# Optimization experiments

Hardware: AMD Instinct MI355X
Metric: run time of the kernel (lower is better)

Reference implementation:

```python
import jax, jax.numpy as jnp
import numpy as np

B, C_IN, C_OUT, IMG, K_STEPS = 32, 64, 8, 128, 8


def setup_inputs() -> dict:
    key = jax.random.key(0)
    k1, k2, k3, k4, k5 = jax.random.split(key, 5)
    x = jax.random.normal(k1, (B, C_IN, IMG, IMG), dtype=jnp.float32)
    rand_pixel = jax.random.uniform(k2, (B, 1, IMG, IMG), dtype=jnp.float32)
    conv_w = jax.random.normal(k3, (C_OUT, C_IN), dtype=jnp.float32) * (1.0 / np.sqrt(C_IN))
    conv_b = jax.random.normal(k4, (C_OUT,), dtype=jnp.float32) * 0.01
    gate = jax.random.normal(k5, (), dtype=jnp.float32)
    # gaussian kernel init: sigma = 1 / (K_steps * log 2)
    log_sigma = jnp.asarray(np.log(1.0 / (K_STEPS * np.log(2.0))), dtype=jnp.float32)
    return {"x": x, "rand_pixel": rand_pixel, "conv_w": conv_w, "conv_b": conv_b,
            "gate": gate, "log_sigma": log_sigma}


def _semiconv(x, conv_w, conv_b, gate):
    # 1x1 conv == channel contraction
    out = gate * (jnp.einsum('oc,bchw->bohw', conv_w, x) + conv_b[None, :, None, None])
    B_, Cout, H, W = out.shape
    g1, g2 = jnp.meshgrid(jnp.linspace(-1.0, 1.0, H), jnp.linspace(-1.0, 1.0, W), indexing='ij')
    coords = jnp.stack([g1, g2])[None].astype(out.dtype)          # [1,2,H,W]
    uv = jnp.concatenate([jnp.zeros((1, Cout - 2, H, W), out.dtype), coords], axis=1)
    return out + uv


def reference(x, rand_pixel, conv_w, conv_b, gate, log_sigma):
    Bsz, _, H, W = x.shape
    feat = _semiconv(x, conv_w, conv_b, gate)              # [B,Cout,H,W]
    Cout = feat.shape[1]
    feat_flat = feat.reshape(Bsz, Cout, H * W)
    sigma = jnp.exp(log_sigma)

    def step(log_scope, _):
        # seed pixel selection: argmax of rand * scope over image
        pixel_probs = rand_pixel * jnp.exp(log_scope)       # [B,1,H,W]
        flat_idx = jnp.argmax(pixel_probs.reshape(Bsz, -1), axis=1)   # [B]
        seed = jnp.take_along_axis(feat_flat, flat_idx[:, None, None], axis=2)  # [B,Cout,1]
        sq_dist = jnp.sum((feat_flat - seed) ** 2, axis=1).reshape(Bsz, 1, H, W)
        alpha = jnp.exp(-sq_dist / sigma)                   # gaussian kernel
        # straight-through clamp to [0.01, 0.99]
        alpha = alpha + jax.lax.stop_gradient(jnp.clip(alpha, 0.01, 0.99) - alpha)
        log_m = log_scope + jnp.log(alpha)
        new_scope = log_scope + jnp.log1p(-alpha)
        return new_scope, (log_m, new_scope)

    log_scope0 = jnp.zeros((Bsz, 1, H, W), feat.dtype)
    final_scope, (lms, lss) = jax.lax.scan(step, log_scope0, None, length=K_STEPS - 1)
    # lms/lss: [K-1,B,1,H,W]
    log_masks = jnp.concatenate([lms, final_scope[None]], axis=0)   # last mask = final scope
    log_scopes = jnp.concatenate([log_scope0[None], lss], axis=0)
    log_masks = jnp.moveaxis(log_masks[:, :, 0], 0, 1)    # [B,K,H,W]
    log_scopes = jnp.moveaxis(log_scopes[:, :, 0], 0, 1)  # [B,K,H,W]
    return log_masks, log_scopes
```

## Files before the change

### kernel.cpp

```cpp
#include <hip/hip_runtime.h>

#define C_IN 64
#define C_OUT 8
#define IMG 128
#define HW (IMG * IMG)
#define BATCH 32
#define K_STEPS 8

#define FEAT_BYTES ((size_t)BATCH * HW * C_OUT * 4)
#define BLK_PER_B 8
#define NFLAGS ((K_STEPS - 1) * BATCH * BLK_PER_B)
#define NSEED0 (BATCH * 16)

union F2U { float2 f2; unsigned long long u; };

__global__ __launch_bounds__(256) void semiconv_kernel(
    const float* __restrict__ x,
    const float* __restrict__ w,
    const float* __restrict__ bias,
    const float* __restrict__ gate_p,
    const float* __restrict__ rand_pixel,
    float* __restrict__ feat,
    unsigned long long* __restrict__ flags,
    unsigned long long* __restrict__ seed0)
{
    __shared__ float sw[C_OUT * C_IN];
    __shared__ float spv[4];
    __shared__ int   spi[4];
    const int tid = threadIdx.x;
    if (blockIdx.x == 0) {
        for (int k = tid; k < NFLAGS; k += 256) flags[k] = 0ULL;
    }
    for (int i = tid; i < C_OUT * C_IN; i += 256) sw[i] = w[i];
    __syncthreads();

    const int b     = blockIdx.x >> 4;
    const int blk16 = blockIdx.x & 15;
    const int p4    = ((blk16 * 256) + tid) * 4;

    const float gate = *gate_p;
    const float* xb = x + (long long)b * C_IN * HW + p4;

    float acc[C_OUT][4];
    #pragma unroll
    for (int o = 0; o < C_OUT; ++o) {
        const float bv = bias[o];
        #pragma unroll
        for (int j = 0; j < 4; ++j) acc[o][j] = bv;
    }

    for (int c = 0; c < C_IN; ++c) {
        const float4 xv = *(const float4*)(xb + c * HW);
        const float xs[4] = {xv.x, xv.y, xv.z, xv.w};
        #pragma unroll
        for (int o = 0; o < C_OUT; ++o) {
            const float wv = sw[o * C_IN + c];
            #pragma unroll
            for (int j = 0; j < 4; ++j) acc[o][j] = fmaf(wv, xs[j], acc[o][j]);
        }
    }

    const int row  = p4 / IMG;
    const int col0 = p4 % IMG;
    const float step = 2.0f / (IMG - 1);
    const float g1 = -1.0f + step * (float)row;

    float* dst = feat + ((long long)b * HW + p4) * C_OUT;
    #pragma unroll
    for (int j = 0; j < 4; ++j) {
        float o0 = gate * acc[0][j];
        float o1 = gate * acc[1][j];
        float o2 = gate * acc[2][j];
        float o3 = gate * acc[3][j];
        float o4 = gate * acc[4][j];
        float o5 = gate * acc[5][j];
        float o6 = gate * acc[6][j] + g1;
        float o7 = gate * acc[7][j] + (-1.0f + step * (float)(col0 + j));
        *(float4*)(dst + j * C_OUT)     = make_float4(o0, o1, o2, o3);
        *(float4*)(dst + j * C_OUT + 4) = make_float4(o4, o5, o6, o7);
    }

    const int lane = tid & 63;
    const int wid  = tid >> 6;
    const float4 rv = *(const float4*)(rand_pixel + (size_t)b * HW + p4);
    float bv = rv.x; int bi = p4;
    if (rv.y > bv) { bv = rv.y; bi = p4 + 1; }
    if (rv.z > bv) { bv = rv.z; bi = p4 + 2; }
    if (rv.w > bv) { bv = rv.w; bi = p4 + 3; }
    #pragma unroll
    for (int off = 1; off < 64; off <<= 1) {
        const float ov = __shfl_xor(bv, off);
        const int   oi = __shfl_xor(bi, off);
        if (ov > bv || (ov == bv && oi < bi)) { bv = ov; bi = oi; }
    }
    if (lane == 0) { spv[wid] = bv; spi[wid] = bi; }
    __syncthreads();
    if (tid == 0) {
        float v = spv[0]; int ix = spi[0];
        #pragma unroll
        for (int wv2 = 1; wv2 < 4; ++wv2) {
            if (spv[wv2] > v || (spv[wv2] == v && spi[wv2] < ix)) { v = spv[wv2]; ix = spi[wv2]; }
        }
        seed0[(b << 4) | blk16] =
            ((unsigned long long)__float_as_uint(v) << 32) |
            (unsigned long long)(unsigned int)ix;
    }
}

#define NT 1024
#define CHUNK (HW / BLK_PER_B)

__device__ __forceinline__ void nt_store2(float* p, float a, float bfl) {
    F2U v; v.f2 = make_float2(a, bfl);
    __builtin_nontemporal_store(v.u, (unsigned long long*)p);
}

__global__ __launch_bounds__(NT) void stick_kernel(
    const float* __restrict__ feat,
    const float* __restrict__ rand_pixel,
    const float* __restrict__ log_sigma_p,
    float* __restrict__ masks,
    float* __restrict__ scopes,
    unsigned long long* __restrict__ flags,
    const unsigned long long* __restrict__ seed0)
{
    const int b    = blockIdx.x & 31;
    const int blk  = blockIdx.x >> 5;
    const int tid  = threadIdx.x;
    const int lane = tid & 63;
    const int wid  = tid >> 6;

    const float inv_sigma = expf(-(*log_sigma_p));

    const float* fb = feat + (size_t)b * HW * C_OUT;
    const float* rb = rand_pixel + (size_t)b * HW;
    float* mb = masks  + (size_t)b * (K_STEPS * HW);
    float* sb = scopes + (size_t)b * (K_STEPS * HW);

    const int p0 = blk * CHUNK + 2 * tid;

    const float4 f0a = *(const float4*)(fb + (size_t)p0 * C_OUT);
    const float4 f0b = *(const float4*)(fb + (size_t)p0 * C_OUT + 4);
    const float4 f1a = *(const float4*)(fb + (size_t)p0 * C_OUT + 8);
    const float4 f1b = *(const float4*)(fb + (size_t)p0 * C_OUT + 12);

    const float2 rr = *(const float2*)(rb + p0);
    float ls0 = 0.0f, ls1 = 0.0f;
    nt_store2(sb + p0, 0.0f, 0.0f);

    __shared__ float swv[2][16];
    __shared__ int   swi[2][16];
    __shared__ int   sSeed[2];

    for (int s = 0; s < K_STEPS - 1; ++s) {
        const int par = s & 1;
        int seedIdx;

        if (s == 0) {
            float gv = -1.0f; int gi = 0x7fffffff;
            if (lane < 16) {
                const unsigned long long got = seed0[(b << 4) | lane];
                gv = __uint_as_float((unsigned int)(got >> 32));
                gi = (int)(unsigned int)(got & 0xffffffffULL);
            }
            #pragma unroll
            for (int off = 1; off < 16; off <<= 1) {
                const float ov = __shfl_xor(gv, off);
                const int   oi = __shfl_xor(gi, off);
                if (ov > gv || (ov == gv && oi < gi)) { gv = ov; gi = oi; }
            }
            seedIdx = __shfl(gi, 0);
        } else {
            const int recbase = (s * BATCH + b) * BLK_PER_B;

            float bv; int bi;
            {
                const float v0 = rr.x * expf(ls0);
                const float v1 = rr.y * expf(ls1);
                bv = v0; bi = p0;
                if (v1 > bv) { bv = v1; bi = p0 + 1; }
            }
            #pragma unroll
            for (int off = 1; off < 64; off <<= 1) {
                const float ov = __shfl_xor(bv, off);
                const int   oi = __shfl_xor(bi, off);
                if (ov > bv || (ov == bv && oi < bi)) { bv = ov; bi = oi; }
            }
            if (lane == 0) { swv[par][wid] = bv; swi[par][wid] = bi; }
            __syncthreads();

            if (wid == 0) {
                float v = (lane < 16) ? swv[par][lane] : -1.0f;
                int   ix = (lane < 16) ? swi[par][lane] : 0x7fffffff;
                #pragma unroll
                for (int off = 1; off < 16; off <<= 1) {
                    const float ov = __shfl_xor(v, off);
                    const int   oi = __shfl_xor(ix, off);
                    if (ov > v || (ov == v && oi < ix)) { v = ov; ix = oi; }
                }
                if (lane == 0) {
                    const unsigned long long pk =
                        ((unsigned long long)__float_as_uint(v) << 32) |
                        (unsigned long long)(unsigned int)(ix + 1);
                    __hip_atomic_store(&flags[recbase + blk], pk,
                                       __ATOMIC_RELAXED, __HIP_MEMORY_SCOPE_AGENT);
                }
                float gv = -1.0f; int gi = 0x7fffffff;
                if (lane < BLK_PER_B) {
                    unsigned long long got;
                    do {
                        got = __hip_atomic_load(&flags[recbase + lane],
                                                __ATOMIC_RELAXED,
                                                __HIP_MEMORY_SCOPE_AGENT);
                    } while (got == 0ULL);
                    gv = __uint_as_float((unsigned int)(got >> 32));
                    gi = (int)(unsigned int)(got & 0xffffffffULL) - 1;
                }
                #pragma unroll
                for (int off = 1; off < 8; off <<= 1) {
                    const float ov = __shfl_xor(gv, off);
                    const int   oi = __shfl_xor(gi, off);
                    if (ov > gv || (ov == gv && oi < gi)) { gv = ov; gi = oi; }
                }
                if (lane == 0) sSeed[par] = gi;
            }
            __syncthreads();
            seedIdx = sSeed[par];
        }

        const float4 s0 = *(const float4*)(fb + (size_t)seedIdx * C_OUT);
        const float4 s1 = *(const float4*)(fb + (size_t)seedIdx * C_OUT + 4);

        float sq0 = 0.0f, sq1 = 0.0f, d;
        d = f0a.x - s0.x; sq0 += d * d;
        d = f0a.y - s0.y; sq0 += d * d;
        d = f0a.z - s0.z; sq0 += d * d;
        d = f0a.w - s0.w; sq0 += d * d;
        d = f0b.x - s1.x; sq0 += d * d;
        d = f0b.y - s1.y; sq0 += d * d;
        d = f0b.z - s1.z; sq0 += d * d;
        d = f0b.w - s1.w; sq0 += d * d;
        d = f1a.x - s0.x; sq1 += d * d;
        d = f1a.y - s0.y; sq1 += d * d;
        d = f1a.z - s0.z; sq1 += d * d;
        d = f1a.w - s0.w; sq1 += d * d;
        d = f1b.x - s1.x; sq1 += d * d;
        d = f1b.y - s1.y; sq1 += d * d;
        d = f1b.z - s1.z; sq1 += d * d;
        d = f1b.w - s1.w; sq1 += d * d;

        float m0, m1;
        {
            const float t = sq0 * inv_sigma;
            float alpha = expf(-t);
            float log_a;
            if (alpha >= 0.99f)      { alpha = 0.99f; log_a = -0.010050336f; }
            else if (alpha <= 0.01f) { alpha = 0.01f; log_a = -4.6051702f;  }
            else                     { log_a = -t; }
            m0 = ls0 + log_a;
            ls0 += log1pf(-alpha);
        }
        {
            const float t = sq1 * inv_sigma;
            float alpha = expf(-t);
            float log_a;
            if (alpha >= 0.99f)      { alpha = 0.99f; log_a = -0.010050336f; }
            else if (alpha <= 0.01f) { alpha = 0.01f; log_a = -4.6051702f;  }
            else                     { log_a = -t; }
            m1 = ls1 + log_a;
            ls1 += log1pf(-alpha);
        }
        nt_store2(mb + s * HW + p0, m0, m1);
        nt_store2(sb + (s + 1) * HW + p0, ls0, ls1);
    }

    nt_store2(mb + (K_STEPS - 1) * HW + p0, ls0, ls1);
}

extern "C" void kernel_launch(void* const* d_in, const int* in_sizes, int n_in,
                              void* d_out, int out_size, void* d_ws, size_t ws_size,
                              hipStream_t stream) {
    const float* x          = (const float*)d_in[0];
    const float* rand_pixel = (const float*)d_in[1];
    const float* conv_w     = (const float*)d_in[2];
    const float* conv_b     = (const float*)d_in[3];
    const float* gate       = (const float*)d_in[4];
    const float* log_sigma  = (const float*)d_in[5];

    float* masks  = (float*)d_out;
    float* scopes = masks + (long long)BATCH * K_STEPS * HW;

    float* feat = (float*)d_ws;
    unsigned long long* flags =
        (unsigned long long*)((char*)d_ws + FEAT_BYTES);
    unsigned long long* seed0 = flags + NFLAGS;

    semiconv_kernel<<<(BATCH * HW) / (256 * 4), 256, 0, stream>>>(
        x, conv_w, conv_b, gate, rand_pixel, feat, flags, seed0);

    stick_kernel<<<BATCH * BLK_PER_B, NT, 0, stream>>>(
        feat, rand_pixel, log_sigma, masks, scopes, flags, seed0);
}
```

Baseline: 72.64 us.

## Replace block barriers with per-round LDS flag spinning and hoist seed argmax

```diff
diff --git a/kernel.cpp b/kernel.cpp
--- a/kernel.cpp
+++ b/kernel.cpp
@@ -9,10 +9,17 @@
 
 #define FEAT_BYTES ((size_t)BATCH * HW * C_OUT * 4)
 #define BLK_PER_B 8
-#define NFLAGS ((K_STEPS - 1) * BATCH * BLK_PER_B)
-#define NSEED0 (BATCH * 16)
+#define NROUNDS (K_STEPS - 1)
+#define NFLAGS (NROUNDS * BATCH * BLK_PER_B)
+#define NT 1024
+#define NW (NT / 64)
+#define CHUNK (HW / BLK_PER_B)
 
 union F2U { float2 f2; unsigned long long u; };
+__device__ __forceinline__ void nt_store2(float* p, float a, float b2) {
+    F2U v; v.f2 = make_float2(a, b2);
+    __builtin_nontemporal_store(v.u, (unsigned long long*)p);
+}
 
 __global__ __launch_bounds__(256) void semiconv_kernel(
     const float* __restrict__ x,
@@ -32,11 +39,38 @@
         for (int k = tid; k < NFLAGS; k += 256) flags[k] = 0ULL;
     }
     for (int i = tid; i < C_OUT * C_IN; i += 256) sw[i] = w[i];
-    __syncthreads();
 
     const int b     = blockIdx.x >> 4;
     const int blk16 = blockIdx.x & 15;
     const int p4    = ((blk16 * 256) + tid) * 4;
+    const int lane  = tid & 63;
+    const int wid   = tid >> 6;
+
+    {
+        const float4 rv = *(const float4*)(rand_pixel + (size_t)b * HW + p4);
+        float bv = rv.x; int bi = p4;
+        if (rv.y > bv) { bv = rv.y; bi = p4 + 1; }
+        if (rv.z > bv) { bv = rv.z; bi = p4 + 2; }
+        if (rv.w > bv) { bv = rv.w; bi = p4 + 3; }
+        #pragma unroll
+        for (int off = 1; off < 64; off <<= 1) {
+            const float ov = __shfl_xor(bv, off);
+            const int   oi = __shfl_xor(bi, off);
+            if (ov > bv || (ov == bv && oi < bi)) { bv = ov; bi = oi; }
+        }
+        if (lane == 0) { spv[wid] = bv; spi[wid] = bi; }
+    }
+    __syncthreads();
+    if (tid == 0) {
+        float v = spv[0]; int ix = spi[0];
+        #pragma unroll
+        for (int wv2 = 1; wv2 < 4; ++wv2) {
+            if (spv[wv2] > v || (spv[wv2] == v && spi[wv2] < ix)) { v = spv[wv2]; ix = spi[wv2]; }
+        }
+        seed0[(b << 4) | blk16] =
+            ((unsigned long long)__float_as_uint(v) << 32) |
+            (unsigned long long)(unsigned int)ix;
+    }
 
     const float gate = *gate_p;
     const float* xb = x + (long long)b * C_IN * HW + p4;
@@ -79,40 +113,6 @@
         *(float4*)(dst + j * C_OUT)     = make_float4(o0, o1, o2, o3);
         *(float4*)(dst + j * C_OUT + 4) = make_float4(o4, o5, o6, o7);
     }
-
-    const int lane = tid & 63;
-    const int wid  = tid >> 6;
-    const float4 rv = *(const float4*)(rand_pixel + (size_t)b * HW + p4);
-    float bv = rv.x; int bi = p4;
-    if (rv.y > bv) { bv = rv.y; bi = p4 + 1; }
-    if (rv.z > bv) { bv = rv.z; bi = p4 + 2; }
-    if (rv.w > bv) { bv = rv.w; bi = p4 + 3; }
-    #pragma unroll
-    for (int off = 1; off < 64; off <<= 1) {
-        const float ov = __shfl_xor(bv, off);
-        const int   oi = __shfl_xor(bi, off);
-        if (ov > bv || (ov == bv && oi < bi)) { bv = ov; bi = oi; }
-    }
-    if (lane == 0) { spv[wid] = bv; spi[wid] = bi; }
-    __syncthreads();
-    if (tid == 0) {
-        float v = spv[0]; int ix = spi[0];
-        #pragma unroll
-        for (int wv2 = 1; wv2 < 4; ++wv2) {
-            if (spv[wv2] > v || (spv[wv2] == v && spi[wv2] < ix)) { v = spv[wv2]; ix = spi[wv2]; }
-        }
-        seed0[(b << 4) | blk16] =
-            ((unsigned long long)__float_as_uint(v) << 32) |
-            (unsigned long long)(unsigned int)ix;
-    }
-}
-
-#define NT 1024
-#define CHUNK (HW / BLK_PER_B)
-
-__device__ __forceinline__ void nt_store2(float* p, float a, float bfl) {
-    F2U v; v.f2 = make_float2(a, bfl);
-    __builtin_nontemporal_store(v.u, (unsigned long long*)p);
 }
 
 __global__ __launch_bounds__(NT) void stick_kernel(
@@ -130,6 +130,20 @@
     const int lane = tid & 63;
     const int wid  = tid >> 6;
 
+    __shared__ unsigned int pv[NROUNDS][NW];
+    __shared__ unsigned int pi[NROUNDS][NW];
+    __shared__ unsigned int sp[NROUNDS];
+
+    {
+        const int total = NROUNDS * NW * 2 + NROUNDS;
+        if (tid < total) {
+            if (tid < NROUNDS * NW)            pv[tid / NW][tid % NW] = 0u;
+            else if (tid < 2 * NROUNDS * NW)   { const int t = tid - NROUNDS * NW; pi[t / NW][t % NW] = 0u; }
+            else                               sp[tid - 2 * NROUNDS * NW] = 0u;
+        }
+    }
+    __syncthreads();
+
     const float inv_sigma = expf(-(*log_sigma_p));
 
     const float* fb = feat + (size_t)b * HW * C_OUT;
@@ -148,12 +162,7 @@
     float ls0 = 0.0f, ls1 = 0.0f;
     nt_store2(sb + p0, 0.0f, 0.0f);
 
-    __shared__ float swv[2][16];
-    __shared__ int   swi[2][16];
-    __shared__ int   sSeed[2];
-
-    for (int s = 0; s < K_STEPS - 1; ++s) {
-        const int par = s & 1;
+    for (int s = 0; s < NROUNDS; ++s) {
         int seedIdx;
 
         if (s == 0) {
@@ -186,12 +195,27 @@
                 const int   oi = __shfl_xor(bi, off);
                 if (ov > bv || (ov == bv && oi < bi)) { bv = ov; bi = oi; }
             }
-            if (lane == 0) { swv[par][wid] = bv; swi[par][wid] = bi; }
-            __syncthreads();
+            if (lane == 0) {
+                __hip_atomic_store(&pv[s][wid], __float_as_uint(bv),
+                                   __ATOMIC_RELAXED, __HIP_MEMORY_SCOPE_WORKGROUP);
+                __hip_atomic_store(&pi[s][wid], (unsigned int)(bi + 1),
+                                   __ATOMIC_RELEASE, __HIP_MEMORY_SCOPE_WORKGROUP);
+            }
 
             if (wid == 0) {
-                float v = (lane < 16) ? swv[par][lane] : -1.0f;
-                int   ix = (lane < 16) ? swi[par][lane] : 0x7fffffff;
+                float v = -1.0f; int ix = 0x7fffffff;
+                if (lane < NW) {
+                    unsigned int f;
+                    do {
+                        f = __hip_atomic_load(&pi[s][lane],
+                                              __ATOMIC_ACQUIRE, __HIP_MEMORY_SCOPE_WORKGROUP);
+                    } while (f == 0u);
+                    const unsigned int vb =
+                        __hip_atomic_load(&pv[s][lane],
+                                          __ATOMIC_RELAXED, __HIP_MEMORY_SCOPE_WORKGROUP);
+                    v = __uint_as_float(vb);
+                    ix = (int)f - 1;
+                }
                 #pragma unroll
                 for (int off = 1; off < 16; off <<= 1) {
                     const float ov = __shfl_xor(v, off);
@@ -222,10 +246,17 @@
                     const int   oi = __shfl_xor(gi, off);
                     if (ov > gv || (ov == gv && oi < gi)) { gv = ov; gi = oi; }
                 }
-                if (lane == 0) sSeed[par] = gi;
-            }
-            __syncthreads();
-            seedIdx = sSeed[par];
+                if (lane == 0) {
+                    __hip_atomic_store(&sp[s], (unsigned int)(gi + 1),
+                                       __ATOMIC_RELEASE, __HIP_MEMORY_SCOPE_WORKGROUP);
+                }
+            }
+            unsigned int sv;
+            do {
+                sv = __hip_atomic_load(&sp[s],
+                                       __ATOMIC_ACQUIRE, __HIP_MEMORY_SCOPE_WORKGROUP);
+            } while (sv == 0u);
+            seedIdx = (int)sv - 1;
         }
 
         const float4 s0 = *(const float4*)(fb + (size_t)seedIdx * C_OUT);
```

After: 74.08 us. About the same (+2.0%).

## Double stick-kernel blocks per batch to one pixel per thread; hoist seed argmax

Applied to the files above, without the earlier changes.

```diff
diff --git a/kernel.cpp b/kernel.cpp
--- a/kernel.cpp
+++ b/kernel.cpp
@@ -8,11 +8,12 @@
 #define K_STEPS 8
 
 #define FEAT_BYTES ((size_t)BATCH * HW * C_OUT * 4)
-#define BLK_PER_B 8
-#define NFLAGS ((K_STEPS - 1) * BATCH * BLK_PER_B)
-#define NSEED0 (BATCH * 16)
-
-union F2U { float2 f2; unsigned long long u; };
+#define BLK_PER_B 16
+#define NROUNDS (K_STEPS - 1)
+#define NFLAGS (NROUNDS * BATCH * BLK_PER_B)
+#define NT 1024
+#define NW (NT / 64)
+#define CHUNK (HW / BLK_PER_B)
 
 __global__ __launch_bounds__(256) void semiconv_kernel(
     const float* __restrict__ x,
@@ -32,11 +33,38 @@
         for (int k = tid; k < NFLAGS; k += 256) flags[k] = 0ULL;
     }
     for (int i = tid; i < C_OUT * C_IN; i += 256) sw[i] = w[i];
-    __syncthreads();
 
     const int b     = blockIdx.x >> 4;
     const int blk16 = blockIdx.x & 15;
     const int p4    = ((blk16 * 256) + tid) * 4;
+    const int lane  = tid & 63;
+    const int wid   = tid >> 6;
+
+    {
+        const float4 rv = *(const float4*)(rand_pixel + (size_t)b * HW + p4);
+        float bv = rv.x; int bi = p4;
+        if (rv.y > bv) { bv = rv.y; bi = p4 + 1; }
+        if (rv.z > bv) { bv = rv.z; bi = p4 + 2; }
+        if (rv.w > bv) { bv = rv.w; bi = p4 + 3; }
+        #pragma unroll
+        for (int off = 1; off < 64; off <<= 1) {
+            const float ov = __shfl_xor(bv, off);
+            const int   oi = __shfl_xor(bi, off);
+            if (ov > bv || (ov == bv && oi < bi)) { bv = ov; bi = oi; }
+        }
+        if (lane == 0) { spv[wid] = bv; spi[wid] = bi; }
+    }
+    __syncthreads();
+    if (tid == 0) {
+        float v = spv[0]; int ix = spi[0];
+        #pragma unroll
+        for (int wv2 = 1; wv2 < 4; ++wv2) {
+            if (spv[wv2] > v || (spv[wv2] == v && spi[wv2] < ix)) { v = spv[wv2]; ix = spi[wv2]; }
+        }
+        seed0[(b << 4) | blk16] =
+            ((unsigned long long)__float_as_uint(v) << 32) |
+            (unsigned long long)(unsigned int)ix;
+    }
 
     const float gate = *gate_p;
     const float* xb = x + (long long)b * C_IN * HW + p4;
@@ -79,43 +107,9 @@
         *(float4*)(dst + j * C_OUT)     = make_float4(o0, o1, o2, o3);
         *(float4*)(dst + j * C_OUT + 4) = make_float4(o4, o5, o6, o7);
     }
-
-    const int lane = tid & 63;
-    const int wid  = tid >> 6;
-    const float4 rv = *(const float4*)(rand_pixel + (size_t)b * HW + p4);
-    float bv = rv.x; int bi = p4;
-    if (rv.y > bv) { bv = rv.y; bi = p4 + 1; }
-    if (rv.z > bv) { bv = rv.z; bi = p4 + 2; }
-    if (rv.w > bv) { bv = rv.w; bi = p4 + 3; }
-    #pragma unroll
-    for (int off = 1; off < 64; off <<= 1) {
-        const float ov = __shfl_xor(bv, off);
-        const int   oi = __shfl_xor(bi, off);
-        if (ov > bv || (ov == bv && oi < bi)) { bv = ov; bi = oi; }
-    }
-    if (lane == 0) { spv[wid] = bv; spi[wid] = bi; }
-    __syncthreads();
-    if (tid == 0) {
-        float v = spv[0]; int ix = spi[0];
-        #pragma unroll
-        for (int wv2 = 1; wv2 < 4; ++wv2) {
-            if (spv[wv2] > v || (spv[wv2] == v && spi[wv2] < ix)) { v = spv[wv2]; ix = spi[wv2]; }
-        }
-        seed0[(b << 4) | blk16] =
-            ((unsigned long long)__float_as_uint(v) << 32) |
-            (unsigned long long)(unsigned int)ix;
-    }
 }
 
-#define NT 1024
-#define CHUNK (HW / BLK_PER_B)
-
-__device__ __forceinline__ void nt_store2(float* p, float a, float bfl) {
-    F2U v; v.f2 = make_float2(a, bfl);
-    __builtin_nontemporal_store(v.u, (unsigned long long*)p);
-}
-
-__global__ __launch_bounds__(NT) void stick_kernel(
+__global__ __launch_bounds__(NT, 8) void stick_kernel(
     const float* __restrict__ feat,
     const float* __restrict__ rand_pixel,
     const float* __restrict__ log_sigma_p,
@@ -137,22 +131,20 @@
     float* mb = masks  + (size_t)b * (K_STEPS * HW);
     float* sb = scopes + (size_t)b * (K_STEPS * HW);
 
-    const int p0 = blk * CHUNK + 2 * tid;
-
-    const float4 f0a = *(const float4*)(fb + (size_t)p0 * C_OUT);
-    const float4 f0b = *(const float4*)(fb + (size_t)p0 * C_OUT + 4);
-    const float4 f1a = *(const float4*)(fb + (size_t)p0 * C_OUT + 8);
-    const float4 f1b = *(const float4*)(fb + (size_t)p0 * C_OUT + 12);
-
-    const float2 rr = *(const float2*)(rb + p0);
-    float ls0 = 0.0f, ls1 = 0.0f;
-    nt_store2(sb + p0, 0.0f, 0.0f);
-
-    __shared__ float swv[2][16];
-    __shared__ int   swi[2][16];
+    const int p0 = blk * CHUNK + tid;
+
+    const float4 fa = *(const float4*)(fb + (size_t)p0 * C_OUT);
+    const float4 fc = *(const float4*)(fb + (size_t)p0 * C_OUT + 4);
+
+    const float rr = rb[p0];
+    float ls0 = 0.0f;
+    __builtin_nontemporal_store(0.0f, sb + p0);
+
+    __shared__ float swv[2][NW];
+    __shared__ int   swi[2][NW];
     __shared__ int   sSeed[2];
 
-    for (int s = 0; s < K_STEPS - 1; ++s) {
+    for (int s = 0; s < NROUNDS; ++s) {
         const int par = s & 1;
         int seedIdx;
 
@@ -173,13 +165,8 @@
         } else {
             const int recbase = (s * BATCH + b) * BLK_PER_B;
 
-            float bv; int bi;
-            {
-                const float v0 = rr.x * expf(ls0);
-                const float v1 = rr.y * expf(ls1);
-                bv = v0; bi = p0;
-                if (v1 > bv) { bv = v1; bi = p0 + 1; }
-            }
+            float bv = rr * expf(ls0);
+            int   bi = p0;
             #pragma unroll
             for (int off = 1; off < 64; off <<= 1) {
                 const float ov = __shfl_xor(bv, off);
@@ -190,8 +177,8 @@
             __syncthreads();
 
             if (wid == 0) {
-                float v = (lane < 16) ? swv[par][lane] : -1.0f;
-                int   ix = (lane < 16) ? swi[par][lane] : 0x7fffffff;
+                float v = (lane < NW) ? swv[par][lane] : -1.0f;
+                int   ix = (lane < NW) ? swi[par][lane] : 0x7fffffff;
                 #pragma unroll
                 for (int off = 1; off < 16; off <<= 1) {
                     const float ov = __shfl_xor(v, off);
@@ -217,7 +204,7 @@
                     gi = (int)(unsigned int)(got & 0xffffffffULL) - 1;
                 }
                 #pragma unroll
-                for (int off = 1; off < 8; off <<= 1) {
+                for (int off = 1; off < 16; off <<= 1) {
                     const float ov = __shfl_xor(gv, off);
                     const int   oi = __shfl_xor(gi, off);
                     if (ov > gv || (ov == gv && oi < gi)) { gv = ov; gi = oi; }
@@ -231,50 +218,30 @@
         const float4 s0 = *(const float4*)(fb + (size_t)seedIdx * C_OUT);
         const float4 s1 = *(const float4*)(fb + (size_t)seedIdx * C_OUT + 4);
 
-        float sq0 = 0.0f, sq1 = 0.0f, d;
-        d = f0a.x - s0.x; sq0 += d * d;
-        d = f0a.y - s0.y; sq0 += d * d;
-        d = f0a.z - s0.z; sq0 += d * d;
-        d = f0a.w - s0.w; sq0 += d * d;
-        d = f0b.x - s1.x; sq0 += d * d;
-        d = f0b.y - s1.y; sq0 += d * d;
-        d = f0b.z - s1.z; sq0 += d * d;
-        d = f0b.w - s1.w; sq0 += d * d;
-        d = f1a.x - s0.x; sq1 += d * d;
-        d = f1a.y - s0.y; sq1 += d * d;
-        d = f1a.z - s0.z; sq1 += d * d;
-        d = f1a.w - s0.w; sq1 += d * d;
-        d = f1b.x - s1.x; sq1 += d * d;
-        d = f1b.y - s1.y; sq1 += d * d;
-        d = f1b.z - s1.z; sq1 += d * d;
-        d = f1b.w - s1.w; sq1 += d * d;
-
-        float m0, m1;
-        {
-            const float t = sq0 * inv_sigma;
-            float alpha = expf(-t);
-            float log_a;
-            if (alpha >= 0.99f)      { alpha = 0.99f; log_a = -0.010050336f; }
-            else if (alpha <= 0.01f) { alpha = 0.01f; log_a = -4.6051702f;  }
-            else                     { log_a = -t; }
-            m0 = ls0 + log_a;
-            ls0 += log1pf(-alpha);
-        }
-        {
-            const float t = sq1 * inv_sigma;
-            float alpha = expf(-t);
-            float log_a;
-            if (alpha >= 0.99f)      { alpha = 0.99f; log_a = -0.010050336f; }
-            else if (alpha <= 0.01f) { alpha = 0.01f; log_a = -4.6051702f;  }
-            else                     { log_a = -t; }
-            m1 = ls1 + log_a;
-            ls1 += log1pf(-alpha);
-        }
-        nt_store2(mb + s * HW + p0, m0, m1);
-        nt_store2(sb + (s + 1) * HW + p0, ls0, ls1);
-    }
-
-    nt_store2(mb + (K_STEPS - 1) * HW + p0, ls0, ls1);
+        float sq0 = 0.0f, d;
+        d = fa.x - s0.x; sq0 += d * d;
+        d = fa.y - s0.y; sq0 += d * d;
+        d = fa.z - s0.z; sq0 += d * d;
+        d = fa.w - s0.w; sq0 += d * d;
+        d = fc.x - s1.x; sq0 += d * d;
+        d = fc.y - s1.y; sq0 += d * d;
+        d = fc.z - s1.z; sq0 += d * d;
+        d = fc.w - s1.w; sq0 += d * d;
+
+        const float t = sq0 * inv_sigma;
+        float alpha = expf(-t);
+        float log_a;
+        if (alpha >= 0.99f)      { alpha = 0.99f; log_a = -0.010050336f; }
+        else if (alpha <= 0.01f) { alpha = 0.01f; log_a = -4.6051702f;  }
+        else                     { log_a = -t; }
+        const float m0 = ls0 + log_a;
+        ls0 += log1pf(-alpha);
+
+        __builtin_nontemporal_store(m0,  mb + s * HW + p0);
+        __builtin_nontemporal_store(ls0, sb + (s + 1) * HW + p0);
+    }
+
+    __builtin_nontemporal_store(ls0, mb + (K_STEPS - 1) * HW + p0);
 }
 
 extern "C" void kernel_launch(void* const* d_in, const int* in_sizes, int n_in,
```

New measurement: 76.21 us. 4.9% more time.
